# Kernel optimization log

Hardware: AMD Instinct MI355X
Metric: run time of the kernel (lower is better)

The kernel has to match this reference:

```python
import jax, jax.numpy as jnp
import numpy as np

D_MODEL = 1024
HEADS = 16
HEAD_DIM = D_MODEL // HEADS
EPS = 1e-6


def feature_map(x):
    # F.elu(x) + 1
    return jax.nn.elu(x) + 1.0


def setup_inputs() -> dict:
    key = jax.random.key(0)
    ks = jax.random.split(key, 9)
    B, N, D = 4, 4096, D_MODEL
    s = 1.0 / np.sqrt(D)
    return {
        "x": jax.random.normal(ks[0], (B, N, D), dtype=jnp.float32),
        "Wq": jax.random.normal(ks[1], (D, D), dtype=jnp.float32) * s,
        "bq": jnp.zeros((D,), dtype=jnp.float32),
        "Wk": jax.random.normal(ks[2], (D, D), dtype=jnp.float32) * s,
        "bk": jnp.zeros((D,), dtype=jnp.float32),
        "Wv": jax.random.normal(ks[3], (D, D), dtype=jnp.float32) * s,
        "bv": jnp.zeros((D,), dtype=jnp.float32),
        "Wo": jax.random.normal(ks[4], (D, D), dtype=jnp.float32) * s,
        "bo": jnp.zeros((D,), dtype=jnp.float32),
    }


def reference(x, Wq, bq, Wk, bk, Wv, bv, Wo, bo):
    B, N, D = x.shape
    H, hd = HEADS, HEAD_DIM
    # torch Linear: y = x @ W.T + b
    q = feature_map((x @ Wq.T + bq).reshape(B, N, H, hd))
    k = feature_map((x @ Wk.T + bk).reshape(B, N, H, hd))
    v = (x @ Wv.T + bv).reshape(B, N, H, hd)
    k_sum = k.sum(axis=1)                                   # (B, H, hd)
    D_inv = 1.0 / (jnp.einsum('bnhd,bhd->bnh', q, k_sum) + EPS)
    context = jnp.einsum('bnhd,bnhv->bhdv', k, v)            # (B, H, hd, hd)
    out = jnp.einsum('bnhd,bhdv->bnhv', q, context) * D_inv[..., None]
    out = out.reshape(B, N, D)
    return out @ Wo.T + bo
```

## Files before the change

kernel.cpp:

```cpp
#include <hip/hip_runtime.h>
#include <hip/hip_bf16.h>

typedef __attribute__((ext_vector_type(8))) short bf16x8;
typedef __attribute__((ext_vector_type(4))) float f32x4;

__device__ __forceinline__ float b2f(unsigned short u) {
  union { unsigned int i; float f; } x; x.i = ((unsigned int)u) << 16; return x.f;
}
__device__ __forceinline__ unsigned short f2b(float f) {
  union { __hip_bfloat16 h; unsigned short u; } x; x.h = __float2bfloat16(f); return x.u;
}
__device__ __forceinline__ f32x4 mfma16(bf16x8 a, bf16x8 b, f32x4 c) {
  return __builtin_amdgcn_mfma_f32_16x16x32_bf16(a, b, c, 0, 0, 0);
}
__device__ __forceinline__ void gl16(const void* g, void* l) {
  __builtin_amdgcn_global_load_lds(
      (const __attribute__((address_space(1))) unsigned int*)g,
      (__attribute__((address_space(3))) unsigned int*)l, 16, 0, 0);
}

__global__ __launch_bounds__(256) void cast_k(const float* __restrict__ src,
                                              unsigned short* __restrict__ dst, int n4) {
  int i = blockIdx.x * 256 + threadIdx.x;
  if (i >= n4) return;
  float4 v = ((const float4*)src)[i];
  ushort4 o;
  o.x = f2b(v.x); o.y = f2b(v.y); o.z = f2b(v.z); o.w = f2b(v.w);
  ((ushort4*)dst)[i] = o;
}

#define BARX() asm volatile("s_barrier" ::: "memory")
#define LGKM0() asm volatile("s_waitcnt lgkmcnt(0)" ::: "memory")
#define WAITV4() asm volatile("s_waitcnt vmcnt(4)" ::: "memory")
#define WAITV0() asm volatile("s_waitcnt vmcnt(0)" ::: "memory")
#define P1() __builtin_amdgcn_s_setprio(1)
#define P0() __builtin_amdgcn_s_setprio(0)

#define STAGE_A(BUF, G, TAU) do { \
  gl16(gA_0 + (size_t)(G) * 65536 + (TAU) * 64, sAB + (BUF) * 32768 + (G) * 16384 + u0 * 16); \
  gl16(gA_1 + (size_t)(G) * 65536 + (TAU) * 64, sAB + (BUF) * 32768 + (G) * 16384 + u1 * 16); } while (0)
#define STAGE_B(BUF, G, TAU) do { \
  gl16(gB_0 + (size_t)(G) * 32768 + (TAU) * 64, sAB + 65536 + (BUF) * 32768 + (G) * 16384 + u0 * 16); \
  gl16(gB_1 + (size_t)(G) * 32768 + (TAU) * 64, sAB + 65536 + (BUF) * 32768 + (G) * 16384 + u1 * 16); } while (0)

#define LOAD_A(BUF, MH) do { \
  _Pragma("unroll") for (int mi = 0; mi < 4; ++mi) { \
    const char* p_ = (const char*)sAB + (BUF) * 32768 + (MH) * 16384 + aRd + mi * 2048; \
    af[mi][0] = *(const bf16x8*)(p_ + sr0); \
    af[mi][1] = *(const bf16x8*)(p_ + sr1); } } while (0)
#define LOAD_B(BUF, NH, DST) do { \
  _Pragma("unroll") for (int ni = 0; ni < 2; ++ni) { \
    const char* p_ = (const char*)sAB + 65536 + (BUF) * 32768 + (NH) * 16384 + bRd + ni * 2048; \
    DST[ni][0] = *(const bf16x8*)(p_ + sr0); \
    DST[ni][1] = *(const bf16x8*)(p_ + sr1); } } while (0)

#define QUAD(MH, NH, BF) do { \
  _Pragma("unroll") for (int mi = 0; mi < 4; ++mi) \
    _Pragma("unroll") for (int ni = 0; ni < 2; ++ni) { \
      acc[(MH) * 4 + mi][(NH) * 2 + ni] = mfma16(af[mi][0], BF[ni][0], acc[(MH) * 4 + mi][(NH) * 2 + ni]); \
      acc[(MH) * 4 + mi][(NH) * 2 + ni] = mfma16(af[mi][1], BF[ni][1], acc[(MH) * 4 + mi][(NH) * 2 + ni]); } } while (0)

template<int MODE>
__global__ __launch_bounds__(512, 2) void gemm256(
    const unsigned short* __restrict__ A,
    const unsigned short* __restrict__ W0, const unsigned short* __restrict__ W1,
    const unsigned short* __restrict__ W2,
    const float* __restrict__ bias0, const float* __restrict__ bias1, const float* __restrict__ bias2,
    float* __restrict__ outF,
    unsigned short* __restrict__ o0, unsigned short* __restrict__ o1, unsigned short* __restrict__ o2,
    int tiles_m, float* __restrict__ ksum)
{
  __shared__ char sAB[131072];
  int bid = blockIdx.x;
  int nwg = gridDim.x;
  int cpx = nwg >> 3;
  int sbid = (bid & 7) * cpx + (bid >> 3);
  int tm = sbid % tiles_m, tn = sbid / tiles_m;
  int m0 = tm * 256, n0 = tn * 256;

  const unsigned short* W = W0; const float* bias = bias0; unsigned short* outB = o0;
  int sel = 0;
  if (MODE == 1) {
    sel = n0 >> 10;
    if (sel == 1) { W = W1; bias = bias1; outB = o1; }
    else if (sel == 2) { W = W2; bias = bias2; outB = o2; }
  }
  int nloc0 = (MODE == 1) ? (n0 & 1023) : n0;

  int t = threadIdx.x, w = t >> 6, l = t & 63;
  int wm = w >> 2, wn = w & 3;

  int u0 = t, u1 = t + 512;
  int lr0 = u0 >> 3, lr1 = u1 >> 3;
  int sl0 = (u0 & 7) ^ (lr0 & 7), sl1 = (u1 & 7) ^ (lr1 & 7);
  int rA0 = ((lr0 >> 6) << 7) + (lr0 & 63), rA1 = ((lr1 >> 6) << 7) + (lr1 & 63);
  int rB0 = ((lr0 >> 5) << 6) + (lr0 & 31), rB1 = ((lr1 >> 5) << 6) + (lr1 & 31);
  const unsigned short* gA_0 = A + (size_t)(m0 + rA0) * 1024 + sl0 * 8;
  const unsigned short* gA_1 = A + (size_t)(m0 + rA1) * 1024 + sl1 * 8;
  const unsigned short* gB_0 = W + (size_t)(nloc0 + rB0) * 1024 + sl0 * 8;
  const unsigned short* gB_1 = W + (size_t)(nloc0 + rB1) * 1024 + sl1 * 8;

  int aRd = (wm * 64 + (l & 15)) * 128;
  int bRd = (wn * 32 + (l & 15)) * 128;
  int sr0 = (((l >> 4) + 0) ^ (l & 7)) * 16;
  int sr1 = (((l >> 4) + 4) ^ (l & 7)) * 16;

  f32x4 acc[8][4];
  f32x4 zero = {0.f, 0.f, 0.f, 0.f};
#pragma unroll
  for (int i = 0; i < 8; ++i)
#pragma unroll
    for (int jx = 0; jx < 4; ++jx) acc[i][jx] = zero;
  bf16x8 af[4][2], bf0[2][2], bf1[2][2];

  STAGE_A(0, 0, 0); STAGE_B(0, 0, 0); STAGE_A(0, 1, 0); STAGE_B(0, 1, 0);
  STAGE_A(1, 0, 1); STAGE_B(1, 0, 1);
  WAITV4();
  BARX();

  for (int j = 0; j < 8; ++j) {
    int t1 = 2 * j + 1;
    int t2 = (j < 7) ? (2 * j + 2) : 14;
    int t3 = (j < 7) ? (2 * j + 3) : 15;
    LOAD_A(0, 0); LOAD_B(0, 0, bf0);
    STAGE_A(1, 1, t1);
    BARX(); LGKM0(); P1(); QUAD(0, 0, bf0); P0(); BARX();
    LOAD_B(0, 1, bf1);
    STAGE_B(1, 1, t1);
    BARX(); LGKM0(); P1(); QUAD(0, 1, bf1); P0(); BARX();
    LOAD_A(0, 1);
    STAGE_A(0, 0, t2);
    BARX(); LGKM0(); P1(); QUAD(1, 0, bf0); P0(); BARX();
    STAGE_B(0, 0, t2);
    BARX(); LGKM0(); P1(); QUAD(1, 1, bf1); P0(); WAITV4(); BARX();
    LOAD_A(1, 0); LOAD_B(1, 0, bf0);
    STAGE_A(0, 1, t2);
    BARX(); LGKM0(); P1(); QUAD(0, 0, bf0); P0(); BARX();
    LOAD_B(1, 1, bf1);
    STAGE_B(0, 1, t2);
    BARX(); LGKM0(); P1(); QUAD(0, 1, bf1); P0(); BARX();
    LOAD_A(1, 1);
    STAGE_A(1, 0, t3);
    BARX(); LGKM0(); P1(); QUAD(1, 0, bf0); P0(); BARX();
    STAGE_B(1, 0, t3);
    BARX(); LGKM0(); P1(); QUAD(1, 1, bf1); P0(); WAITV4(); BARX();
  }
  WAITV0();

  if (MODE == 1 && sel >= 1) {
    int b_idx = m0 >> 12;
    int nloc_h = nloc0 >> 6;
#pragma unroll
    for (int mq = 0; mq < 8; ++mq) {
      int r_base = wm * 128 + (mq >> 2) * 64 + (mq & 3) * 16 + ((l >> 4) << 2);
#pragma unroll
      for (int nq = 0; nq < 4; ++nq) {
        int c_loc = wn * 64 + (nq >> 1) * 32 + (nq & 1) * 16 + (l & 15);
        float bb = bias[nloc0 + c_loc];
        float v0 = acc[mq][nq][0] + bb, v1 = acc[mq][nq][1] + bb;
        float v2 = acc[mq][nq][2] + bb, v3 = acc[mq][nq][3] + bb;
        if (sel == 1) {
          v0 = (v0 > 0.0f) ? (v0 + 1.0f) : __expf(v0);
          v1 = (v1 > 0.0f) ? (v1 + 1.0f) : __expf(v1);
          v2 = (v2 > 0.0f) ? (v2 + 1.0f) : __expf(v2);
          v3 = (v3 > 0.0f) ? (v3 + 1.0f) : __expf(v3);
        }
        unsigned long long pk =
            (unsigned long long)(f2b(v0) | ((unsigned int)f2b(v1) << 16)) |
            ((unsigned long long)(f2b(v2) | ((unsigned int)f2b(v3) << 16)) << 32);
        int byte = c_loc * 512 + ((r_base * 2) ^ ((c_loc & 7) << 4));
        *(unsigned long long*)(sAB + byte) = pk;
      }
    }
    __syncthreads();
#pragma unroll
    for (int p = 0; p < 4; ++p) {
      int c_loc = p * 64 + w * 8 + (l >> 3);
      int n_off = (l & 7) * 32;
      int d = c_loc & 63;
      int bh = b_idx * 16 + nloc_h + (c_loc >> 6);
      unsigned short* dst = outB + (size_t)(bh * 64 + d) * 4096 + (m0 & 4095) + n_off;
      float s = 0.f;
#pragma unroll
      for (int i = 0; i < 4; ++i) {
        int byte = c_loc * 512 + (((n_off + i * 8) * 2) ^ ((c_loc & 7) << 4));
        bf16x8 ch = *(const bf16x8*)(sAB + byte);
        if (sel == 1) {
#pragma unroll
          for (int jj = 0; jj < 8; ++jj) s += b2f((unsigned short)ch[jj]);
        }
        *(bf16x8*)(dst + i * 8) = ch;
      }
      if (sel == 1) {
        s += __shfl_xor(s, 1);
        s += __shfl_xor(s, 2);
        s += __shfl_xor(s, 4);
        if ((l & 7) == 0) atomicAdd(ksum + bh * 64 + d, s);
      }
    }
  } else {
#pragma unroll
    for (int mq = 0; mq < 8; ++mq) {
      int grow = m0 + wm * 128 + (mq >> 2) * 64 + (mq & 3) * 16 + ((l >> 4) << 2);
#pragma unroll
      for (int nq = 0; nq < 4; ++nq) {
        int gcol = n0 + wn * 64 + (nq >> 1) * 32 + (nq & 1) * 16 + (l & 15);
        if (MODE == 0) {
          float bb = bias[gcol];
#pragma unroll
          for (int r = 0; r < 4; ++r)
            outF[(size_t)(grow + r) * 1024 + gcol] = acc[mq][nq][r] + bb;
        } else {
          int c = gcol & 1023;
          float bb = bias[c];
#pragma unroll
          for (int r = 0; r < 4; ++r) {
            float v = acc[mq][nq][r] + bb;
            v = (v > 0.0f) ? (v + 1.0f) : __expf(v);
            outB[(size_t)(grow + r) * 1024 + c] = f2b(v);
          }
        }
      }
    }
  }
}

__global__ __launch_bounds__(64) void ctx_gemm(
    const unsigned short* __restrict__ vT,
    const unsigned short* __restrict__ kT,
    float* __restrict__ ctxT)
{
  int bid = blockIdx.x;
  int bh = bid >> 3, ch = bid & 7;
  int l = threadIdx.x;
  const unsigned short* aB = vT + ((size_t)bh * 64 + (l & 15)) * 4096 + ch * 512 + ((l >> 4) << 3);
  const unsigned short* bB = kT + ((size_t)bh * 64 + (l & 15)) * 4096 + ch * 512 + ((l >> 4) << 3);
  f32x4 acc[4][4];
  f32x4 zero = {0.f, 0.f, 0.f, 0.f};
#pragma unroll
  for (int i = 0; i < 4; ++i)
#pragma unroll
    for (int j = 0; j < 4; ++j) acc[i][j] = zero;
  for (int ks = 0; ks < 16; ++ks) {
    bf16x8 av[4], bv[4];
#pragma unroll
    for (int mi = 0; mi < 4; ++mi) av[mi] = *(const bf16x8*)(aB + (size_t)mi * 16 * 4096 + ks * 32);
#pragma unroll
    for (int ni = 0; ni < 4; ++ni) bv[ni] = *(const bf16x8*)(bB + (size_t)ni * 16 * 4096 + ks * 32);
#pragma unroll
    for (int mi = 0; mi < 4; ++mi)
#pragma unroll
      for (int ni = 0; ni < 4; ++ni)
        acc[mi][ni] = mfma16(av[mi], bv[ni], acc[mi][ni]);
  }
#pragma unroll
  for (int mi = 0; mi < 4; ++mi)
#pragma unroll
    for (int ni = 0; ni < 4; ++ni)
#pragma unroll
      for (int r = 0; r < 4; ++r) {
        int e = mi * 16 + ((l >> 4) << 2) + r;
        int d = ni * 16 + (l & 15);
        atomicAdd(ctxT + (size_t)bh * 4096 + e * 64 + d, acc[mi][ni][r]);
      }
}

__global__ __launch_bounds__(256) void att_gemm(
    unsigned short* __restrict__ q,
    const float* __restrict__ ctxT,
    const float* __restrict__ ksum)
{
  int bid = blockIdx.x;
  int bh = bid & 63, mt = bid >> 6;
  int b = bh >> 4, h = bh & 15;
  int t = threadIdx.x, w = t >> 6, l = t & 63;
  int m0 = mt * 256 + w * 64;

  bf16x8 bfr[2][4];
  const float* cb = ctxT + (size_t)bh * 4096;
#pragma unroll
  for (int ks = 0; ks < 2; ++ks)
#pragma unroll
    for (int ni = 0; ni < 4; ++ni) {
      const float* p = cb + (ni * 16 + (l & 15)) * 64 + ks * 32 + ((l >> 4) << 3);
#pragma unroll
      for (int j = 0; j < 8; ++j) bfr[ks][ni][j] = (short)f2b(p[j]);
    }

  const float* kp = ksum + bh * 64 + ((l >> 4) << 3);
  float kp0[8], kp1[8];
#pragma unroll
  for (int j = 0; j < 8; ++j) { kp0[j] = kp[j]; kp1[j] = kp[j + 32]; }

  f32x4 acc[4][4];
  f32x4 zero = {0.f, 0.f, 0.f, 0.f};
#pragma unroll
  for (int i = 0; i < 4; ++i)
#pragma unroll
    for (int j = 0; j < 4; ++j) acc[i][j] = zero;
  float dvv[4];

  size_t rowbase = (size_t)(b * 4096 + m0 + (l & 15)) * 1024 + h * 64 + ((l >> 4) << 3);
#pragma unroll
  for (int mi = 0; mi < 4; ++mi) {
    bf16x8 av0 = *(const bf16x8*)(q + rowbase + (size_t)mi * 16 * 1024);
    bf16x8 av1 = *(const bf16x8*)(q + rowbase + (size_t)mi * 16 * 1024 + 32);
    float s = 0.f;
#pragma unroll
    for (int j = 0; j < 8; ++j) {
      s += b2f((unsigned short)av0[j]) * kp0[j];
      s += b2f((unsigned short)av1[j]) * kp1[j];
    }
    s += __shfl_xor(s, 16);
    s += __shfl_xor(s, 32);
    dvv[mi] = 1.0f / (s + 1e-6f);
#pragma unroll
    for (int ni = 0; ni < 4; ++ni) {
      acc[mi][ni] = mfma16(av0, bfr[0][ni], acc[mi][ni]);
      acc[mi][ni] = mfma16(av1, bfr[1][ni], acc[mi][ni]);
    }
  }

#pragma unroll
  for (int mi = 0; mi < 4; ++mi) {
    float sc[4];
#pragma unroll
    for (int r = 0; r < 4; ++r) sc[r] = __shfl(dvv[mi], ((l >> 4) << 2) + r);
#pragma unroll
    for (int ni = 0; ni < 4; ++ni) {
      int e = ni * 16 + (l & 15);
#pragma unroll
      for (int r = 0; r < 4; ++r) {
        int npos = m0 + mi * 16 + ((l >> 4) << 2) + r;
        q[(size_t)(b * 4096 + npos) * 1024 + h * 64 + e] = f2b(acc[mi][ni][r] * sc[r]);
      }
    }
  }
}

extern "C" void kernel_launch(void* const* d_in, const int* in_sizes, int n_in,
                              void* d_out, int out_size, void* d_ws, size_t ws_size,
                              hipStream_t stream)
{
  const float* x  = (const float*)d_in[0];
  const float* bq = (const float*)d_in[2];
  const float* bk = (const float*)d_in[4];
  const float* bv = (const float*)d_in[6];
  const float* bo = (const float*)d_in[8];
  const float* Wq = (const float*)d_in[1];
  const float* Wk = (const float*)d_in[3];
  const float* Wv = (const float*)d_in[5];
  const float* Wo = (const float*)d_in[7];
  float* out = (float*)d_out;

  char* ws = (char*)d_ws;
  const size_t SB = (size_t)16384 * 1024 * 2;
  const size_t NEED = 4 * SB + 4 * (1u << 21) + 2 * (1u << 20) + (1u << 14);
  if (ws_size < NEED) return;

  unsigned short* xb  = (unsigned short*)(ws);
  unsigned short* qb  = (unsigned short*)(ws + SB);
  unsigned short* kTb = (unsigned short*)(ws + 2 * SB);
  unsigned short* vTb = (unsigned short*)(ws + 3 * SB);
  unsigned short* wqb = (unsigned short*)(ws + 4 * SB);
  unsigned short* wkb = (unsigned short*)(ws + 4 * SB + (1u << 21));
  unsigned short* wvb = (unsigned short*)(ws + 4 * SB + (2u << 21));
  unsigned short* wob = (unsigned short*)(ws + 4 * SB + (3u << 21));
  float* ctxT = (float*)(ws + 4 * SB + (4u << 21));
  float* ksum = (float*)(ws + 4 * SB + (4u << 21) + (2u << 20));

  hipMemsetAsync(ctxT, 0, 64 * 64 * 64 * 4, stream);
  hipMemsetAsync(ksum, 0, 64 * 64 * 4, stream);

  cast_k<<<16384, 256, 0, stream>>>(x, xb, 16777216 / 4);
  cast_k<<<1024, 256, 0, stream>>>(Wq, wqb, 1048576 / 4);
  cast_k<<<1024, 256, 0, stream>>>(Wk, wkb, 1048576 / 4);
  cast_k<<<1024, 256, 0, stream>>>(Wv, wvb, 1048576 / 4);
  cast_k<<<1024, 256, 0, stream>>>(Wo, wob, 1048576 / 4);

  gemm256<1><<<768, 512, 0, stream>>>(xb, wqb, wkb, wvb, bq, bk, bv,
                                      nullptr, qb, kTb, vTb, 64, ksum);

  ctx_gemm<<<512, 64, 0, stream>>>(vTb, kTb, ctxT);

  att_gemm<<<1024, 256, 0, stream>>>(qb, ctxT, ksum);

  gemm256<0><<<256, 512, 0, stream>>>(qb, wob, nullptr, nullptr, bo, nullptr, nullptr,
                                      out, nullptr, nullptr, nullptr, 64, nullptr);
}
```

Baseline: 262.4 us.

## Split ctx_gemm reduction across four waves and coalesce transposed K/V stores

ctx_gemm now runs 256 threads per block, with each wave covering a quarter of the 512-token chunk. Partial 64x64 context tiles are combined through padded shared memory, so each element gets one global atomic per block instead of one per wave. In the projection epilogue, the transposed K/V writeback now has 32 lanes cover one row with 16-byte stores, which gives contiguous 512-byte segments instead of strided per-lane 64-byte runs. The k-sum reduction changes to match, with a wider shuffle tree and one atomic per row. The cost is about 66KB of LDS per ctx block, which limits occupancy.

```diff
diff --git a/kernel.cpp b/kernel.cpp
--- a/kernel.cpp
+++ b/kernel.cpp
@@ -174,28 +174,24 @@
     }
     __syncthreads();
 #pragma unroll
-    for (int p = 0; p < 4; ++p) {
-      int c_loc = p * 64 + w * 8 + (l >> 3);
-      int n_off = (l & 7) * 32;
+    for (int qq = 0; qq < 16; ++qq) {
+      int c_loc = qq * 16 + w * 2 + (l >> 5);
+      int n_off = (l & 31) * 8;
       int d = c_loc & 63;
       int bh = b_idx * 16 + nloc_h + (c_loc >> 6);
-      unsigned short* dst = outB + (size_t)(bh * 64 + d) * 4096 + (m0 & 4095) + n_off;
-      float s = 0.f;
-#pragma unroll
-      for (int i = 0; i < 4; ++i) {
-        int byte = c_loc * 512 + (((n_off + i * 8) * 2) ^ ((c_loc & 7) << 4));
-        bf16x8 ch = *(const bf16x8*)(sAB + byte);
-        if (sel == 1) {
-#pragma unroll
-          for (int jj = 0; jj < 8; ++jj) s += b2f((unsigned short)ch[jj]);
-        }
-        *(bf16x8*)(dst + i * 8) = ch;
-      }
+      int byte = c_loc * 512 + ((n_off * 2) ^ ((c_loc & 7) << 4));
+      bf16x8 ch = *(const bf16x8*)(sAB + byte);
+      *(bf16x8*)(outB + (size_t)(bh * 64 + d) * 4096 + (m0 & 4095) + n_off) = ch;
       if (sel == 1) {
+        float s = 0.f;
+#pragma unroll
+        for (int jj = 0; jj < 8; ++jj) s += b2f((unsigned short)ch[jj]);
         s += __shfl_xor(s, 1);
         s += __shfl_xor(s, 2);
         s += __shfl_xor(s, 4);
-        if ((l & 7) == 0) atomicAdd(ksum + bh * 64 + d, s);
+        s += __shfl_xor(s, 8);
+        s += __shfl_xor(s, 16);
+        if ((l & 31) == 0) atomicAdd(ksum + bh * 64 + d, s);
       }
     }
   } else {
@@ -225,23 +221,25 @@
   }
 }
 
-__global__ __launch_bounds__(64) void ctx_gemm(
+__global__ __launch_bounds__(256) void ctx_gemm(
     const unsigned short* __restrict__ vT,
     const unsigned short* __restrict__ kT,
     float* __restrict__ ctxT)
 {
+  __shared__ float red[4][64 * 65];
   int bid = blockIdx.x;
   int bh = bid >> 3, ch = bid & 7;
-  int l = threadIdx.x;
-  const unsigned short* aB = vT + ((size_t)bh * 64 + (l & 15)) * 4096 + ch * 512 + ((l >> 4) << 3);
-  const unsigned short* bB = kT + ((size_t)bh * 64 + (l & 15)) * 4096 + ch * 512 + ((l >> 4) << 3);
+  int t = threadIdx.x, wv = t >> 6, l = t & 63;
+  int noff = ch * 512 + wv * 128 + ((l >> 4) << 3);
+  const unsigned short* aB = vT + ((size_t)bh * 64 + (l & 15)) * 4096 + noff;
+  const unsigned short* bB = kT + ((size_t)bh * 64 + (l & 15)) * 4096 + noff;
   f32x4 acc[4][4];
   f32x4 zero = {0.f, 0.f, 0.f, 0.f};
 #pragma unroll
   for (int i = 0; i < 4; ++i)
 #pragma unroll
     for (int j = 0; j < 4; ++j) acc[i][j] = zero;
-  for (int ks = 0; ks < 16; ++ks) {
+  for (int ks = 0; ks < 4; ++ks) {
     bf16x8 av[4], bv[4];
 #pragma unroll
     for (int mi = 0; mi < 4; ++mi) av[mi] = *(const bf16x8*)(aB + (size_t)mi * 16 * 4096 + ks * 32);
@@ -261,8 +259,14 @@
       for (int r = 0; r < 4; ++r) {
         int e = mi * 16 + ((l >> 4) << 2) + r;
         int d = ni * 16 + (l & 15);
-        atomicAdd(ctxT + (size_t)bh * 4096 + e * 64 + d, acc[mi][ni][r]);
-      }
+        red[wv][e * 65 + d] = acc[mi][ni][r];
+      }
+  __syncthreads();
+  for (int o = t; o < 4096; o += 256) {
+    int idx = (o >> 6) * 65 + (o & 63);
+    float s = red[0][idx] + red[1][idx] + red[2][idx] + red[3][idx];
+    atomicAdd(ctxT + (size_t)bh * 4096 + o, s);
+  }
 }
 
 __global__ __launch_bounds__(256) void att_gemm(
@@ -381,7 +385,7 @@
   gemm256<1><<<768, 512, 0, stream>>>(xb, wqb, wkb, wvb, bq, bk, bv,
                                       nullptr, qb, kTb, vTb, 64, ksum);
 
-  ctx_gemm<<<512, 64, 0, stream>>>(vTb, kTb, ctxT);
+  ctx_gemm<<<512, 256, 0, stream>>>(vTb, kTb, ctxT);
 
   att_gemm<<<1024, 256, 0, stream>>>(qb, ctxT, ksum);
 
```

After: 250.9 us. 4.4% less time.
